# Performance work log

Hardware: AMD Instinct MI355X
Metric: run time of the kernel (lower is better)

The kernel has to match this reference:

```python
import jax, jax.numpy as jnp
import numpy as np

N_NODES = 100000
N_EDGES = 3200000
ALPHA = 0.9
N_LAYERS = 10


def setup_inputs() -> dict:
    key = jax.random.key(0)
    ks = jax.random.split(key, 6)
    x = jax.random.normal(ks[0], (N_NODES, 512), dtype=jnp.float32)
    W_in = jax.random.normal(ks[1], (256, 512), dtype=jnp.float32) * (1.0 / np.sqrt(512))
    b_in = jnp.zeros((256,), dtype=jnp.float32)
    W_out = jax.random.normal(ks[2], (64, 256), dtype=jnp.float32) * (1.0 / np.sqrt(256))
    b_out = jnp.zeros((64,), dtype=jnp.float32)
    edge_index = jax.random.randint(ks[3], (2, N_EDGES), 0, N_NODES, dtype=jnp.int64)
    # ~1/avg_degree scale keeps the iterated propagation numerically stable
    edge_weight = jax.random.uniform(ks[4], (N_EDGES,), dtype=jnp.float32) * (1.0 / 32.0)
    return {"x": x, "W_in": W_in, "b_in": b_in, "W_out": W_out,
            "b_out": b_out, "edge_index": edge_index, "edge_weight": edge_weight}


def _spmm(edge_index, edge_weight, z, n_nodes):
    # out[dst] += w * z[src]  (COO SpMM via gather + segment_sum)
    src, dst = edge_index[0], edge_index[1]
    msg = z[src] * edge_weight[:, None]            # [E, C]
    return jax.ops.segment_sum(msg, dst, num_segments=n_nodes)


def reference(x, W_in, b_in, W_out, b_out, edge_index, edge_weight):
    n_nodes = x.shape[0]
    h = jax.nn.relu(x @ W_in.T + b_in)             # linear_in -> (dropout: eval, identity) -> relu
    z = h @ W_out.T + b_out                        # linear_out: [N, n_classes]
    z0 = z
    for _ in range(N_LAYERS):
        # APPNP propagation: alpha-weighted adj propagation + residual blend with x_0
        z = ALPHA * _spmm(edge_index, edge_weight, z, n_nodes) + (1.0 - ALPHA) * z0
    return z
```

## Files before the change

### kernel.cpp

```cpp
#include <hip/hip_runtime.h>
#include <hip/hip_bf16.h>

typedef __attribute__((ext_vector_type(8))) short bf16x8;
typedef __attribute__((ext_vector_type(4))) float f32x4;

__device__ __forceinline__ short f2b(float f) {
    unsigned u = __builtin_bit_cast(unsigned, f);
    unsigned r = (u + 0x7fffu + ((u >> 16) & 1u)) >> 16;
    return (short)r;
}
__device__ __forceinline__ unsigned f2bu(float f) {
    unsigned u = __builtin_bit_cast(unsigned, f);
    return ((u + 0x7fffu + ((u >> 16) & 1u)) >> 16) & 0xffffu;
}
__device__ __forceinline__ float blo(unsigned u) {
    return __builtin_bit_cast(float, u << 16);
}
__device__ __forceinline__ float bhi(unsigned u) {
    return __builtin_bit_cast(float, u & 0xffff0000u);
}

__global__ __launch_bounds__(256) void fused_linear(
    const float* __restrict__ x, const float* __restrict__ W_in,
    const float* __restrict__ b_in, const float* __restrict__ W_out,
    const float* __restrict__ b_out, unsigned short* __restrict__ z0, int M)
{
    __shared__ __align__(16) char smem[65536];
    short* At = (short*)smem;
    short* Bt = (short*)(smem + 5120);
    short* Wo = (short*)smem;
    short* Hs = (short*)(smem + 32768);

    const int tid  = threadIdx.x;
    const int lane = tid & 63;
    const int w    = tid >> 6;
    const int row0 = blockIdx.x * 64;

    f32x4 acc[16];
#pragma unroll
    for (int t = 0; t < 16; ++t) { acc[t][0]=0.f; acc[t][1]=0.f; acc[t][2]=0.f; acc[t][3]=0.f; }

    const int f4 = tid & 7;
    for (int kk = 0; kk < 16; ++kk) {
        __syncthreads();
#pragma unroll
        for (int p = 0; p < 2; ++p) {
            int row = (tid >> 3) + p * 32;
            int grow = row0 + row;
            float4 v = make_float4(0.f, 0.f, 0.f, 0.f);
            if (grow < M) v = *(const float4*)(x + (size_t)grow * 512 + kk * 32 + f4 * 4);
            short* d = At + row * 40 + f4 * 4;
            d[0] = f2b(v.x); d[1] = f2b(v.y); d[2] = f2b(v.z); d[3] = f2b(v.w);
        }
#pragma unroll
        for (int p = 0; p < 8; ++p) {
            int row = (tid >> 3) + p * 32;
            float4 v = *(const float4*)(W_in + (size_t)row * 512 + kk * 32 + f4 * 4);
            short* d = Bt + row * 40 + f4 * 4;
            d[0] = f2b(v.x); d[1] = f2b(v.y); d[2] = f2b(v.z); d[3] = f2b(v.w);
        }
        __syncthreads();
        bf16x8 a = *(const bf16x8*)(At + (16 * w + (lane & 15)) * 40 + (lane >> 4) * 8);
#pragma unroll
        for (int t = 0; t < 16; ++t) {
            bf16x8 b = *(const bf16x8*)(Bt + (16 * t + (lane & 15)) * 40 + (lane >> 4) * 8);
            acc[t] = __builtin_amdgcn_mfma_f32_16x16x32_bf16(a, b, acc[t], 0, 0, 0);
        }
    }
    __syncthreads();
#pragma unroll
    for (int t = 0; t < 16; ++t) {
        int col = 16 * t + (lane & 15);
        float bv = b_in[col];
        int kk2 = col >> 5, q = (col >> 3) & 3, j = col & 7;
#pragma unroll
        for (int r = 0; r < 4; ++r) {
            int row = 16 * w + (lane >> 4) * 4 + r;
            float h = acc[t][r] + bv;
            h = h > 0.f ? h : 0.f;
            Hs[((kk2 * 4 + q) * 64 + row) * 8 + j] = f2b(h);
        }
    }
#pragma unroll
    for (int p = 0; p < 16; ++p) {
        int idx4 = tid + p * 256;
        int row = idx4 >> 6, c0 = (idx4 & 63) * 4;
        float4 v = *(const float4*)(W_out + row * 256 + c0);
        int kk2 = c0 >> 5, q = (c0 >> 3) & 3, j0 = c0 & 7;
        short* d = Wo + ((kk2 * 4 + q) * 64 + row) * 8 + j0;
        d[0] = f2b(v.x); d[1] = f2b(v.y); d[2] = f2b(v.z); d[3] = f2b(v.w);
    }
    __syncthreads();
    f32x4 acc2[4];
#pragma unroll
    for (int t = 0; t < 4; ++t) { acc2[t][0]=0.f; acc2[t][1]=0.f; acc2[t][2]=0.f; acc2[t][3]=0.f; }
#pragma unroll
    for (int kk2 = 0; kk2 < 8; ++kk2) {
        bf16x8 a = *(const bf16x8*)(Hs + ((kk2 * 4 + (lane >> 4)) * 64 + 16 * w + (lane & 15)) * 8);
#pragma unroll
        for (int t = 0; t < 4; ++t) {
            bf16x8 b = *(const bf16x8*)(Wo + ((kk2 * 4 + (lane >> 4)) * 64 + 16 * t + (lane & 15)) * 8);
            acc2[t] = __builtin_amdgcn_mfma_f32_16x16x32_bf16(a, b, acc2[t], 0, 0, 0);
        }
    }
#pragma unroll
    for (int t = 0; t < 4; ++t) {
        int col = 16 * t + (lane & 15);
        float bv = b_out[col];
#pragma unroll
        for (int r = 0; r < 4; ++r) {
            int grow = row0 + 16 * w + (lane >> 4) * 4 + r;
            if (grow < M) z0[(size_t)grow * 64 + col] = (unsigned short)f2bu(acc2[t][r] + bv);
        }
    }
}

#define CSR_CH   16384
#define MAXBUK   256

__global__ __launch_bounds__(256) void coarse_hist(
    const int* __restrict__ dst, int* __restrict__ M, int E, int nbuk)
{
    __shared__ int cnt[MAXBUK];
    int tid = threadIdx.x, blk = blockIdx.x;
    for (int i = tid; i < nbuk; i += 256) cnt[i] = 0;
    __syncthreads();
    int e0 = blk * CSR_CH, e1 = e0 + CSR_CH; if (e1 > E) e1 = E;
    for (int e = e0 + tid; e < e1; e += 256) atomicAdd(&cnt[dst[e] >> 9], 1);
    __syncthreads();
    for (int i = tid; i < nbuk; i += 256) M[blk * nbuk + i] = cnt[i];
}

__global__ __launch_bounds__(256) void bucket_scan(
    int* __restrict__ M, int* __restrict__ bucketBase, int nblk, int nbuk)
{
    __shared__ int tot[MAXBUK];
    int tid = threadIdx.x;
    for (int r = tid; r < nbuk; r += 256) {
        int s = 0;
        for (int k = 0; k < nblk; ++k) s += M[k * nbuk + r];
        tot[r] = s;
    }
    __syncthreads();
    if (tid == 0) {
        int s = 0;
        for (int r = 0; r < nbuk; ++r) { int t = tot[r]; tot[r] = s; bucketBase[r] = s; s += t; }
        bucketBase[nbuk] = s;
    }
    __syncthreads();
    for (int r = tid; r < nbuk; r += 256) {
        int s = tot[r];
        for (int k = 0; k < nblk; ++k) { int t = M[k * nbuk + r]; M[k * nbuk + r] = s; s += t; }
    }
}

__global__ __launch_bounds__(256) void coarse_scatter(
    const int* __restrict__ src, const int* __restrict__ dst,
    const float* __restrict__ ew, const int* __restrict__ M,
    int4* __restrict__ tmp, int E, int nbuk)
{
    __shared__ int off[MAXBUK];
    int tid = threadIdx.x, blk = blockIdx.x;
    for (int i = tid; i < nbuk; i += 256) off[i] = M[blk * nbuk + i];
    __syncthreads();
    int e0 = blk * CSR_CH, e1 = e0 + CSR_CH; if (e1 > E) e1 = E;
    for (int e = e0 + tid; e < e1; e += 256) {
        int d = dst[e];
        int pos = atomicAdd(&off[d >> 9], 1);
        tmp[pos] = make_int4(src[e], __builtin_bit_cast(int, ew[e]), d, 0);
    }
}

__global__ __launch_bounds__(256) void fine_sort(
    const int4* __restrict__ tmp, const int* __restrict__ bucketBase,
    int2* __restrict__ csr, int* __restrict__ rowptr, int N, int E)
{
    __shared__ int fc[512];
    __shared__ int fo[512];
    __shared__ int wsum[5];
    int b = blockIdx.x, tid = threadIdx.x;
    int base = bucketBase[b], cnt = bucketBase[b + 1] - base;
    int node0 = b << 9;

    fc[tid] = 0; fc[tid + 256] = 0;
    __syncthreads();
    for (int i = tid; i < cnt; i += 256)
        atomicAdd(&fc[tmp[base + i].z - node0], 1);
    __syncthreads();

    int lane = tid & 63, wid = tid >> 6;
    int runbase = 0;
    for (int h = 0; h < 2; ++h) {
        int v = fc[h * 256 + tid];
        int x = v;
#pragma unroll
        for (int off = 1; off < 64; off <<= 1) { int y = __shfl_up(x, off); if (lane >= off) x += y; }
        if (lane == 63) wsum[wid] = x;
        __syncthreads();
        if (tid == 0) { int s = 0; for (int k = 0; k < 4; ++k) { int t = wsum[k]; wsum[k] = s; s += t; } wsum[4] = s; }
        __syncthreads();
        fo[h * 256 + tid] = runbase + wsum[wid] + x - v;
        runbase += wsum[4];
        __syncthreads();
    }

    for (int i = tid; i < 512; i += 256) {
        int node = node0 + i;
        if (node < N) rowptr[node] = base + fo[i];
    }
    if (b == 0 && tid == 0) rowptr[N] = E;
    __syncthreads();

    for (int i = tid; i < cnt; i += 256) {
        int4 ed = tmp[base + i];
        int pos = atomicAdd(&fo[ed.z - node0], 1);
        csr[base + pos] = make_int2(ed.x, ed.y);
    }
}

__global__ __launch_bounds__(256) void prop_kernel(
    const int* __restrict__ rowptr, const int2* __restrict__ csr,
    const unsigned short* __restrict__ zin, const unsigned short* __restrict__ z0,
    unsigned short* __restrict__ zout_b, float* __restrict__ zout_f,
    int n, int final_layer)
{
    int lane = threadIdx.x & 63;
    int node = blockIdx.x * 4 + (threadIdx.x >> 6);
    if (node >= n) return;
    int beg = rowptr[node], end = rowptr[node + 1];
    const int sub = lane >> 3;
    const int k8  = lane & 7;

    float acc[8];
#pragma unroll
    for (int i = 0; i < 8; ++i) acc[i] = 0.f;

    for (int b = beg; b < end; b += 64) {
        int e = b + lane;
        int2 ed = (e < end) ? csr[e] : make_int2(0, 0);
        int cnt = end - b; if (cnt > 64) cnt = 64;
        int groups = (cnt + 7) >> 3;
        for (int j = 0; j < groups; ++j) {
            int idx = j * 8 + sub;
            int sj = __shfl(ed.x, idx);
            int wb = __shfl(ed.y, idx);
            if (idx < cnt) {
                float wj = __builtin_bit_cast(float, wb);
                uint4 v = *(const uint4*)(zin + (size_t)sj * 64 + k8 * 8);
                acc[0] += wj * blo(v.x); acc[1] += wj * bhi(v.x);
                acc[2] += wj * blo(v.y); acc[3] += wj * bhi(v.y);
                acc[4] += wj * blo(v.z); acc[5] += wj * bhi(v.z);
                acc[6] += wj * blo(v.w); acc[7] += wj * bhi(v.w);
            }
        }
    }
#pragma unroll
    for (int off = 8; off < 64; off <<= 1) {
#pragma unroll
        for (int i = 0; i < 8; ++i) acc[i] += __shfl_xor(acc[i], off);
    }
    if (sub == 0) {
        uint4 zv = *(const uint4*)(z0 + (size_t)node * 64 + k8 * 8);
        float o0 = 0.9f * acc[0] + 0.1f * blo(zv.x);
        float o1 = 0.9f * acc[1] + 0.1f * bhi(zv.x);
        float o2 = 0.9f * acc[2] + 0.1f * blo(zv.y);
        float o3 = 0.9f * acc[3] + 0.1f * bhi(zv.y);
        float o4 = 0.9f * acc[4] + 0.1f * blo(zv.z);
        float o5 = 0.9f * acc[5] + 0.1f * bhi(zv.z);
        float o6 = 0.9f * acc[6] + 0.1f * blo(zv.w);
        float o7 = 0.9f * acc[7] + 0.1f * bhi(zv.w);
        if (final_layer) {
            float* dp = zout_f + (size_t)node * 64 + k8 * 8;
            *(float4*)dp       = make_float4(o0, o1, o2, o3);
            *(float4*)(dp + 4) = make_float4(o4, o5, o6, o7);
        } else {
            uint4 pv;
            pv.x = f2bu(o0) | (f2bu(o1) << 16);
            pv.y = f2bu(o2) | (f2bu(o3) << 16);
            pv.z = f2bu(o4) | (f2bu(o5) << 16);
            pv.w = f2bu(o6) | (f2bu(o7) << 16);
            *(uint4*)(zout_b + (size_t)node * 64 + k8 * 8) = pv;
        }
    }
}

static inline size_t align_up(size_t v, size_t a) { return (v + a - 1) & ~(a - 1); }

extern "C" void kernel_launch(void* const* d_in, const int* in_sizes, int n_in,
                              void* d_out, int out_size, void* d_ws, size_t ws_size,
                              hipStream_t stream)
{
    const float* x     = (const float*)d_in[0];
    const float* W_in  = (const float*)d_in[1];
    const float* b_in  = (const float*)d_in[2];
    const float* W_out = (const float*)d_in[3];
    const float* b_out = (const float*)d_in[4];
    const int*   ei    = (const int*)d_in[5];
    const float* ew    = (const float*)d_in[6];

    const int N = in_sizes[0] / 512;
    const int E = in_sizes[6];
    const int* e_src = ei;
    const int* e_dst = ei + E;

    const int nbuk = (N + 511) >> 9;
    const int nblk = (E + CSR_CH - 1) / CSR_CH;

    char* p = (char*)d_ws;
    size_t zbytes = align_up((size_t)N * 64 * sizeof(unsigned short), 256);
    unsigned short* z0b = (unsigned short*)p; p += zbytes;
    int2* csr   = (int2*)p; p += align_up((size_t)E * 8, 256);
    int* rowptr = (int*)p;  p += align_up((size_t)(N + 1) * 4, 256);
    int* M      = (int*)p;  p += align_up((size_t)nblk * nbuk * 4, 256);
    int* bucketBase = (int*)p; p += align_up((size_t)(nbuk + 1) * 4, 256);
    int4* tmp   = (int4*)p; p += align_up((size_t)E * 16, 256);
    unsigned short* zA = (unsigned short*)tmp;
    unsigned short* zB = zA + (size_t)N * 64;

    fused_linear<<<(N + 63) / 64, 256, 0, stream>>>(x, W_in, b_in, W_out, b_out, z0b, N);

    coarse_hist<<<nblk, 256, 0, stream>>>(e_dst, M, E, nbuk);
    bucket_scan<<<1, 256, 0, stream>>>(M, bucketBase, nblk, nbuk);
    coarse_scatter<<<nblk, 256, 0, stream>>>(e_src, e_dst, ew, M, tmp, E, nbuk);
    fine_sort<<<nbuk, 256, 0, stream>>>(tmp, bucketBase, csr, rowptr, N, E);

    float* out_f = (float*)d_out;
    int pgrid = (N + 3) / 4;
    for (int i = 0; i < 10; ++i) {
        const unsigned short* zin = (i == 0) ? z0b : ((i & 1) ? zA : zB);
        unsigned short* zoutb = (i & 1) ? zB : zA;
        prop_kernel<<<pgrid, 256, 0, stream>>>(rowptr, csr, zin, z0b,
                                               zoutb, out_f, N, (i == 9) ? 1 : 0);
    }
}
```

Baseline: 1.231 ms.

## Pre-convert weights to bf16 fragment layout and stream via global_load_lds

Adds a small prep kernel that converts W_in and W_out to bf16 once, already arranged in MFMA fragment order. The MLP kernel then loads W_in tiles straight into LDS with global_load_lds and reads W_out fragments directly from global memory. Before, every block re-read fp32 weights and converted them in its own prologue. LDS use drops from 64KB to about 33KB, which may allow higher occupancy, at the cost of one extra launch and uncached-per-block global reads for W_out.

```diff
diff --git a/kernel.cpp b/kernel.cpp
--- a/kernel.cpp
+++ b/kernel.cpp
@@ -20,75 +20,91 @@
     return __builtin_bit_cast(float, u & 0xffff0000u);
 }
 
-__global__ __launch_bounds__(256) void fused_linear(
-    const float* __restrict__ x, const float* __restrict__ W_in,
-    const float* __restrict__ b_in, const float* __restrict__ W_out,
+__global__ __launch_bounds__(256) void wprep(
+    const float* __restrict__ W_in, const float* __restrict__ W_out,
+    unsigned short* __restrict__ Wi_f, unsigned short* __restrict__ Wo_f)
+{
+    int o = blockIdx.x * 256 + threadIdx.x;
+    if (o < 131072) {
+        int j = o & 7, lane = (o >> 3) & 63, t = (o >> 9) & 15, kk = o >> 13;
+        int n = t * 16 + (lane & 15);
+        int k = kk * 32 + ((lane >> 4) << 3) + j;
+        Wi_f[o] = (unsigned short)f2bu(W_in[n * 512 + k]);
+    } else if (o < 131072 + 16384) {
+        int o2 = o - 131072;
+        int j = o2 & 7, lane = (o2 >> 3) & 63, t = (o2 >> 9) & 3, kk2 = o2 >> 11;
+        int n = t * 16 + (lane & 15);
+        int k = kk2 * 32 + ((lane >> 4) << 3) + j;
+        Wo_f[o2] = (unsigned short)f2bu(W_out[n * 256 + k]);
+    }
+}
+
+__global__ __launch_bounds__(256) void mlp(
+    const float* __restrict__ x, const unsigned short* __restrict__ Wi_f,
+    const float* __restrict__ b_in, const unsigned short* __restrict__ Wo_f,
     const float* __restrict__ b_out, unsigned short* __restrict__ z0, int M)
 {
-    __shared__ __align__(16) char smem[65536];
+    __shared__ __align__(16) char smem[33280];
     short* At = (short*)smem;
     short* Bt = (short*)(smem + 5120);
-    short* Wo = (short*)smem;
-    short* Hs = (short*)(smem + 32768);
+    short* Hs = (short*)smem;
 
     const int tid  = threadIdx.x;
     const int lane = tid & 63;
     const int w    = tid >> 6;
     const int row0 = blockIdx.x * 64;
+    const int c    = lane & 15;
+    const int qk   = lane >> 4;
 
     f32x4 acc[16];
 #pragma unroll
     for (int t = 0; t < 16; ++t) { acc[t][0]=0.f; acc[t][1]=0.f; acc[t][2]=0.f; acc[t][3]=0.f; }
 
-    const int f4 = tid & 7;
+    const int f4   = tid & 7;
+    const int arow = tid >> 3;
     for (int kk = 0; kk < 16; ++kk) {
         __syncthreads();
 #pragma unroll
         for (int p = 0; p < 2; ++p) {
-            int row = (tid >> 3) + p * 32;
+            int row = arow + p * 32;
             int grow = row0 + row;
             float4 v = make_float4(0.f, 0.f, 0.f, 0.f);
             if (grow < M) v = *(const float4*)(x + (size_t)grow * 512 + kk * 32 + f4 * 4);
-            short* d = At + row * 40 + f4 * 4;
-            d[0] = f2b(v.x); d[1] = f2b(v.y); d[2] = f2b(v.z); d[3] = f2b(v.w);
-        }
-#pragma unroll
-        for (int p = 0; p < 8; ++p) {
-            int row = (tid >> 3) + p * 32;
-            float4 v = *(const float4*)(W_in + (size_t)row * 512 + kk * 32 + f4 * 4);
-            short* d = Bt + row * 40 + f4 * 4;
-            d[0] = f2b(v.x); d[1] = f2b(v.y); d[2] = f2b(v.z); d[3] = f2b(v.w);
-        }
-        __syncthreads();
-        bf16x8 a = *(const bf16x8*)(At + (16 * w + (lane & 15)) * 40 + (lane >> 4) * 8);
+            uint2 pk;
+            pk.x = f2bu(v.x) | (f2bu(v.y) << 16);
+            pk.y = f2bu(v.z) | (f2bu(v.w) << 16);
+            *(uint2*)(At + row * 40 + f4 * 4) = pk;
+        }
+#pragma unroll
+        for (int i = 0; i < 4; ++i) {
+            int t = w * 4 + i;
+            const unsigned short* g = Wi_f + (((size_t)kk * 16 + t) * 64 + lane) * 8;
+            __builtin_amdgcn_global_load_lds(
+                (const __attribute__((address_space(1))) unsigned int*)g,
+                (__attribute__((address_space(3))) unsigned int*)(Bt + t * 512),
+                16, 0, 0);
+        }
+        __syncthreads();
+        bf16x8 a = *(const bf16x8*)(At + (16 * w + c) * 40 + qk * 8);
 #pragma unroll
         for (int t = 0; t < 16; ++t) {
-            bf16x8 b = *(const bf16x8*)(Bt + (16 * t + (lane & 15)) * 40 + (lane >> 4) * 8);
+            bf16x8 b = *(const bf16x8*)(Bt + (t * 64 + lane) * 8);
             acc[t] = __builtin_amdgcn_mfma_f32_16x16x32_bf16(a, b, acc[t], 0, 0, 0);
         }
     }
     __syncthreads();
 #pragma unroll
     for (int t = 0; t < 16; ++t) {
-        int col = 16 * t + (lane & 15);
+        int col = 16 * t + c;
         float bv = b_in[col];
-        int kk2 = col >> 5, q = (col >> 3) & 3, j = col & 7;
+        int qb = col >> 3, j = col & 7;
 #pragma unroll
         for (int r = 0; r < 4; ++r) {
-            int row = 16 * w + (lane >> 4) * 4 + r;
+            int row = 16 * w + qk * 4 + r;
             float h = acc[t][r] + bv;
             h = h > 0.f ? h : 0.f;
-            Hs[((kk2 * 4 + q) * 64 + row) * 8 + j] = f2b(h);
-        }
-    }
-#pragma unroll
-    for (int p = 0; p < 16; ++p) {
-        int idx4 = tid + p * 256;
-        int row = idx4 >> 6, c0 = (idx4 & 63) * 4;
-        float4 v = *(const float4*)(W_out + row * 256 + c0);
-        int kk2 = c0 >> 5, q = (c0 >> 3) & 3, j0 = c0 & 7;
-        short* d = Wo + ((kk2 * 4 + q) * 64 + row) * 8 + j0;
-        d[0] = f2b(v.x); d[1] = f2b(v.y); d[2] = f2b(v.z); d[3] = f2b(v.w);
+            Hs[qb * 520 + row * 8 + j] = f2b(h);
+        }
     }
     __syncthreads();
     f32x4 acc2[4];
@@ -96,20 +112,20 @@
     for (int t = 0; t < 4; ++t) { acc2[t][0]=0.f; acc2[t][1]=0.f; acc2[t][2]=0.f; acc2[t][3]=0.f; }
 #pragma unroll
     for (int kk2 = 0; kk2 < 8; ++kk2) {
-        bf16x8 a = *(const bf16x8*)(Hs + ((kk2 * 4 + (lane >> 4)) * 64 + 16 * w + (lane & 15)) * 8);
+        bf16x8 a2 = *(const bf16x8*)(Hs + (kk2 * 4 + qk) * 520 + (16 * w + c) * 8);
 #pragma unroll
         for (int t = 0; t < 4; ++t) {
-            bf16x8 b = *(const bf16x8*)(Wo + ((kk2 * 4 + (lane >> 4)) * 64 + 16 * t + (lane & 15)) * 8);
-            acc2[t] = __builtin_amdgcn_mfma_f32_16x16x32_bf16(a, b, acc2[t], 0, 0, 0);
+            bf16x8 b2 = *(const bf16x8*)(Wo_f + (((size_t)kk2 * 4 + t) * 64 + lane) * 8);
+            acc2[t] = __builtin_amdgcn_mfma_f32_16x16x32_bf16(a2, b2, acc2[t], 0, 0, 0);
         }
     }
 #pragma unroll
     for (int t = 0; t < 4; ++t) {
-        int col = 16 * t + (lane & 15);
+        int col = 16 * t + c;
         float bv = b_out[col];
 #pragma unroll
         for (int r = 0; r < 4; ++r) {
-            int grow = row0 + 16 * w + (lane >> 4) * 4 + r;
+            int grow = row0 + 16 * w + qk * 4 + r;
             if (grow < M) z0[(size_t)grow * 64 + col] = (unsigned short)f2bu(acc2[t][r] + bv);
         }
     }
@@ -309,6 +325,8 @@
     char* p = (char*)d_ws;
     size_t zbytes = align_up((size_t)N * 64 * sizeof(unsigned short), 256);
     unsigned short* z0b = (unsigned short*)p; p += zbytes;
+    unsigned short* Wi_f = (unsigned short*)p; p += align_up(131072 * 2, 256);
+    unsigned short* Wo_f = (unsigned short*)p; p += align_up(16384 * 2, 256);
     int2* csr   = (int2*)p; p += align_up((size_t)E * 8, 256);
     int* rowptr = (int*)p;  p += align_up((size_t)(N + 1) * 4, 256);
     int* M      = (int*)p;  p += align_up((size_t)nblk * nbuk * 4, 256);
@@ -317,7 +335,8 @@
     unsigned short* zA = (unsigned short*)tmp;
     unsigned short* zB = zA + (size_t)N * 64;
 
-    fused_linear<<<(N + 63) / 64, 256, 0, stream>>>(x, W_in, b_in, W_out, b_out, z0b, N);
+    wprep<<<(131072 + 16384 + 255) / 256, 256, 0, stream>>>(W_in, W_out, Wi_f, Wo_f);
+    mlp<<<(N + 63) / 64, 256, 0, stream>>>(x, Wi_f, b_in, Wo_f, b_out, z0b, N);
 
     coarse_hist<<<nblk, 256, 0, stream>>>(e_dst, M, E, nbuk);
     bucket_scan<<<1, 256, 0, stream>>>(M, bucketBase, nblk, nbuk);
```

New measurement: 1.181 ms. 1.04x faster.
